# Performance work log

Measured on AMD Instinct MI355X. Metric: run time of the kernel, lower is better.

## Reference

```python
import jax, jax.numpy as jnp
import numpy as np

SLOPE = 5.0                # surrogate gradient slope (SurrogateGradient default)
REFRACTORY_PERIOD = 2.0    # config.refractory_period
ADAPT_DECAY = 0.9          # threshold_adapt EMA decay
ADAPT_INC = 0.1


@jax.custom_vjp
def spike_fn(membrane, threshold):
    # Heaviside spike with surrogate gradient (fast sigmoid), matching SurrogateGradient
    return (membrane >= threshold).astype(membrane.dtype)

def _spike_fwd(membrane, threshold):
    return spike_fn(membrane, threshold), (membrane, threshold)

def _spike_bwd(res, g):
    membrane, threshold = res
    s = jax.nn.sigmoid(SLOPE * (membrane - threshold))
    grad_m = g * SLOPE * s * (1.0 - s)
    # torch returns None (zero) grad for threshold through the spike op itself
    return grad_m, jnp.zeros_like(threshold)

spike_fn.defvjp(_spike_fwd, _spike_bwd)


def setup_inputs() -> dict:
    key = jax.random.key(0)
    kx, = jax.random.split(key, 1)
    B, S, D = 16, 2048, 1024
    x = jax.random.normal(kx, (B, S, D), dtype=jnp.float32)
    beta_mem = jnp.asarray(0.9, dtype=jnp.float32)                      # membrane_decay
    beta_syn = jnp.exp(jnp.asarray(-1.0 / 5.0, dtype=jnp.float32))      # exp(-1/tau_syn)
    threshold_adapt_p = jnp.full((1,), 0.1, dtype=jnp.float32)          # nn.Parameter ones(1)*0.1
    threshold_scale = jnp.ones((D,), dtype=jnp.float32)
    learnable_threshold = jnp.ones((D,), dtype=jnp.float32)             # threshold=1.0
    return {
        "x": x,
        "beta_mem": beta_mem,
        "beta_syn": beta_syn,
        "threshold_adapt_p": threshold_adapt_p,
        "threshold_scale": threshold_scale,
        "learnable_threshold": learnable_threshold,
    }


def _lif(x, beta_mem, beta_syn, threshold_adapt_p, threshold_scale, learnable_threshold):
    B, S, D = x.shape
    z = jnp.zeros((B, D), dtype=x.dtype)
    init = (z, z, z, z)  # membrane, synaptic, threshold_adapt, refractory

    def step(carry, xt):  # xt: (B, D)
        membrane, synaptic, th_adapt, refractory = carry
        synaptic = beta_syn * synaptic + xt
        non_refractory = (refractory <= 0).astype(x.dtype)
        membrane = beta_mem * membrane + synaptic * non_refractory
        cur_th = learnable_threshold + threshold_adapt_p * th_adapt * threshold_scale
        spikes = spike_fn(membrane, cur_th)
        membrane = membrane - spikes * cur_th  # reset_mode='subtract'
        th_adapt = ADAPT_DECAY * th_adapt + ADAPT_INC * spikes
        refractory = jnp.where(
            spikes > 0.5,
            jnp.full_like(spikes, REFRACTORY_PERIOD),
            jnp.clip(refractory - 1.0, 0.0),
        )
        return (membrane, synaptic, th_adapt, refractory), spikes

    carry, spikes = jax.lax.scan(step, init, jnp.swapaxes(x, 0, 1))  # scan over seq
    spike_train = jnp.swapaxes(spikes, 0, 1)  # (B, S, D)
    return spike_train, carry


def reference(x, beta_mem, beta_syn, threshold_adapt_p, threshold_scale, learnable_threshold):
    spike_train, (membrane, synaptic, th_adapt, refractory) = _lif(
        x, beta_mem, beta_syn, threshold_adapt_p, threshold_scale, learnable_threshold
    )
    return spike_train, membrane, synaptic, th_adapt, refractory
```

## Files before the change

### kernel.cpp

```cpp
#include <hip/hip_runtime.h>
#include <stdint.h>


#define SB 16
#define SS 2048
#define SD 1024
#define TILE 64
#define NT (SS / TILE)

typedef const __attribute__((address_space(1))) void* gas_ptr;
typedef __attribute__((address_space(3))) void* las_ptr;

__global__ __launch_bounds__(128, 1) void lif_kernel(
    const float* __restrict__ x,
    const float* __restrict__ beta_mem_p,
    const float* __restrict__ beta_syn_p,
    const float* __restrict__ adapt_p,
    const float* __restrict__ scale_p,
    const float* __restrict__ lth_p,
    float* __restrict__ out)
{
#pragma clang fp contract(off)
    __shared__ __attribute__((aligned(16))) float xbuf[3][TILE][64];
    __shared__ float sbuf[2][64][TILE + 1];

    const int bk = blockIdx.x;
    const int b  = bk >> 4;
    const int d0 = (bk & 15) << 6;

    if (threadIdx.x < 64) {
        const int lane = threadIdx.x;
        const int d    = d0 + lane;

        const float beta_mem = beta_mem_p[0];
        const float beta_syn = beta_syn_p[0];
        const float p        = adapt_p[0];
        const float scale    = scale_p[d];
        const float lth      = lth_p[d];

        float mem = 0.f, syn = 0.f, tha = 0.f;
        bool  nref = true;
        bool  f1 = false, f2 = false;

        __syncthreads();

        int cbuf = 0;
        for (int k = 0; k < NT; ++k) {
            const int sb = k & 1;

            float xa[16], xbv[16], xc[16], xd[16];
            #pragma unroll
            for (int i = 0; i < 16; ++i) xa[i]  = xbuf[cbuf][i][lane];
            #pragma unroll
            for (int i = 0; i < 16; ++i) xbv[i] = xbuf[cbuf][16 + i][lane];
            #pragma unroll
            for (int i = 0; i < 16; ++i) xc[i]  = xbuf[cbuf][32 + i][lane];
            #pragma unroll
            for (int i = 0; i < 16; ++i) xd[i]  = xbuf[cbuf][48 + i][lane];

            auto step = [&](float xt, int ti) {
                syn = __builtin_fmaf(beta_syn, syn, xt);
                const float syn_eff = nref ? syn : 0.f;
                mem = __builtin_fmaf(beta_mem, mem, syn_eff);
                const float q      = p * tha;
                const float cur_th = __builtin_fmaf(q, scale, lth);
                const bool  fired  = (mem >= cur_th);
                const float spike  = fired ? 1.f : 0.f;
                mem = mem - (fired ? cur_th : 0.f);
                tha = __builtin_fmaf(0.9f, tha, fired ? 0.1f : 0.f);
                nref = !(fired || f1);
                f2 = f1; f1 = fired;
                sbuf[sb][lane][ti] = spike;
            };

            #pragma unroll
            for (int i = 0; i < 16; ++i) step(xa[i], i);
            #pragma unroll
            for (int i = 0; i < 16; ++i) step(xbv[i], 16 + i);
            #pragma unroll
            for (int i = 0; i < 16; ++i) step(xc[i], 32 + i);
            #pragma unroll
            for (int i = 0; i < 16; ++i) step(xd[i], 48 + i);

            __syncthreads();
            cbuf = (cbuf == 2) ? 0 : cbuf + 1;
        }

        const float refr = f1 ? 2.0f : (f2 ? 1.0f : 0.0f);
        const size_t base = (size_t)SB * SS * SD;
        const size_t off  = (size_t)b * SD + d;
        out[base + 0 * (size_t)SB * SD + off] = mem;
        out[base + 1 * (size_t)SB * SD + off] = syn;
        out[base + 2 * (size_t)SB * SD + off] = tha;
        out[base + 3 * (size_t)SB * SD + off] = refr;
    } else {
        const int hl = threadIdx.x - 64;

        const float* xb   = x   + ((size_t)b * SS) * SD + d0;
        float*       outb = out + ((size_t)b * SS) * SD + d0;

        const int srow = hl >> 4;
        const int scol = (hl & 15) << 2;
        const float* src_base = xb + (size_t)srow * SD + scol;

        auto issue_tile = [&](int k, int buf) {
            const float* s0 = src_base + (size_t)(k * TILE) * SD;
            float* dst = &xbuf[buf][0][0];
            #pragma unroll
            for (int r = 0; r < 16; ++r) {
                __builtin_amdgcn_global_load_lds(
                    (gas_ptr)(s0 + (size_t)(r * 4) * SD),
                    (las_ptr)(dst + r * 4 * 64),
                    16, 0, 0);
            }
        };

        auto store_tile = [&](int tk) {
            const int sb = tk & 1;
            int idx = tk * TILE * SD + hl;
            #pragma unroll 8
            for (int t = 0; t < TILE; ++t) {
                outb[idx] = sbuf[sb][hl][t];
                idx += SD;
            }
        };

        issue_tile(0, 0);
        issue_tile(1, 1);
        __syncthreads();

        int nbuf = 2;
        for (int k = 0; k < NT; ++k) {
            if (k + 2 < NT) {
                issue_tile(k + 2, nbuf);
                nbuf = (nbuf == 2) ? 0 : nbuf + 1;
            }
            if (k >= 1) store_tile(k - 1);
            __syncthreads();
        }
        store_tile(NT - 1);
    }
}

extern "C" void kernel_launch(void* const* d_in, const int* in_sizes, int n_in,
                              void* d_out, int out_size, void* d_ws, size_t ws_size,
                              hipStream_t stream) {
    const float* x        = (const float*)d_in[0];
    const float* beta_mem = (const float*)d_in[1];
    const float* beta_syn = (const float*)d_in[2];
    const float* adapt_p  = (const float*)d_in[3];
    const float* scale    = (const float*)d_in[4];
    const float* lth      = (const float*)d_in[5];
    float* out = (float*)d_out;

    lif_kernel<<<256, 128, 0, stream>>>(x, beta_mem, beta_syn, adapt_p, scale, lth, out);
}
```

Before: 79.49 us.

## Run two interleaved LIF chains per lane and store spikes directly from compute wave

Each compute lane now advances two independent neuron chains, giving the scan instruction-level parallelism across adjacent D columns. The grid is halved to 128 blocks of 128 columns each. The LDS spike staging buffer and the loader wave's store loop are removed, so the compute wave writes float2 spikes straight to global memory. The loader adds explicit vmcnt waits before barriers. This trades half the blocks (fewer CUs in use on a 256-CU part) for more ILP per serial chain, and it puts global stores on the critical compute wave.

```diff
diff --git a/kernel.cpp b/kernel.cpp
--- a/kernel.cpp
+++ b/kernel.cpp
@@ -11,6 +11,12 @@
 typedef const __attribute__((address_space(1))) void* gas_ptr;
 typedef __attribute__((address_space(3))) void* las_ptr;
 
+struct Chain {
+    float mem, syn, tha;
+    bool  nref, f1, f2;
+    float scale, lth;
+};
+
 __global__ __launch_bounds__(128, 1) void lif_kernel(
     const float* __restrict__ x,
     const float* __restrict__ beta_mem_p,
@@ -21,112 +27,100 @@
     float* __restrict__ out)
 {
 #pragma clang fp contract(off)
-    __shared__ __attribute__((aligned(16))) float xbuf[3][TILE][64];
-    __shared__ float sbuf[2][64][TILE + 1];
+    __shared__ __attribute__((aligned(16))) float xbuf[3][TILE][128];
 
     const int bk = blockIdx.x;
-    const int b  = bk >> 4;
-    const int d0 = (bk & 15) << 6;
+    const int b  = bk >> 3;
+    const int d0 = (bk & 7) << 7;
 
     if (threadIdx.x < 64) {
         const int lane = threadIdx.x;
-        const int d    = d0 + lane;
+        const int dA   = d0 + 2 * lane;
+        const int dB   = dA + 1;
 
         const float beta_mem = beta_mem_p[0];
         const float beta_syn = beta_syn_p[0];
         const float p        = adapt_p[0];
-        const float scale    = scale_p[d];
-        const float lth      = lth_p[d];
 
-        float mem = 0.f, syn = 0.f, tha = 0.f;
-        bool  nref = true;
-        bool  f1 = false, f2 = false;
+        Chain c0{0.f, 0.f, 0.f, true, false, false, scale_p[dA], lth_p[dA]};
+        Chain c1{0.f, 0.f, 0.f, true, false, false, scale_p[dB], lth_p[dB]};
+
+        float2* out2 = (float2*)(out + ((size_t)b * SS) * SD + d0);
+        int sidx = lane;
+
+        auto step = [&](float xt, Chain& c) -> float {
+            c.syn = __builtin_fmaf(beta_syn, c.syn, xt);
+            const float syn_eff = c.nref ? c.syn : 0.f;
+            c.mem = __builtin_fmaf(beta_mem, c.mem, syn_eff);
+            const float q      = p * c.tha;
+            const float cur_th = __builtin_fmaf(q, c.scale, c.lth);
+            const bool  fired  = (c.mem >= cur_th);
+            const float spike  = fired ? 1.f : 0.f;
+            c.mem = c.mem - (fired ? cur_th : 0.f);
+            c.tha = __builtin_fmaf(0.9f, c.tha, fired ? 0.1f : 0.f);
+            c.nref = !(fired || c.f1);
+            c.f2 = c.f1; c.f1 = fired;
+            return spike;
+        };
 
         __syncthreads();
 
         int cbuf = 0;
         for (int k = 0; k < NT; ++k) {
-            const int sb = k & 1;
-
-            float xa[16], xbv[16], xc[16], xd[16];
+            float2 xa[16];
             #pragma unroll
-            for (int i = 0; i < 16; ++i) xa[i]  = xbuf[cbuf][i][lane];
-            #pragma unroll
-            for (int i = 0; i < 16; ++i) xbv[i] = xbuf[cbuf][16 + i][lane];
-            #pragma unroll
-            for (int i = 0; i < 16; ++i) xc[i]  = xbuf[cbuf][32 + i][lane];
-            #pragma unroll
-            for (int i = 0; i < 16; ++i) xd[i]  = xbuf[cbuf][48 + i][lane];
-
-            auto step = [&](float xt, int ti) {
-                syn = __builtin_fmaf(beta_syn, syn, xt);
-                const float syn_eff = nref ? syn : 0.f;
-                mem = __builtin_fmaf(beta_mem, mem, syn_eff);
-                const float q      = p * tha;
-                const float cur_th = __builtin_fmaf(q, scale, lth);
-                const bool  fired  = (mem >= cur_th);
-                const float spike  = fired ? 1.f : 0.f;
-                mem = mem - (fired ? cur_th : 0.f);
-                tha = __builtin_fmaf(0.9f, tha, fired ? 0.1f : 0.f);
-                nref = !(fired || f1);
-                f2 = f1; f1 = fired;
-                sbuf[sb][lane][ti] = spike;
-            };
-
-            #pragma unroll
-            for (int i = 0; i < 16; ++i) step(xa[i], i);
-            #pragma unroll
-            for (int i = 0; i < 16; ++i) step(xbv[i], 16 + i);
-            #pragma unroll
-            for (int i = 0; i < 16; ++i) step(xc[i], 32 + i);
-            #pragma unroll
-            for (int i = 0; i < 16; ++i) step(xd[i], 48 + i);
-
+            for (int g = 0; g < 4; ++g) {
+                #pragma unroll
+                for (int i = 0; i < 16; ++i)
+                    xa[i] = *(const float2*)&xbuf[cbuf][g * 16 + i][2 * lane];
+                #pragma unroll
+                for (int i = 0; i < 16; ++i) {
+                    float2 sv;
+                    sv.x = step(xa[i].x, c0);
+                    sv.y = step(xa[i].y, c1);
+                    out2[sidx] = sv;
+                    sidx += SD / 2;
+                }
+            }
             __syncthreads();
             cbuf = (cbuf == 2) ? 0 : cbuf + 1;
         }
 
-        const float refr = f1 ? 2.0f : (f2 ? 1.0f : 0.0f);
+        const float r0 = c0.f1 ? 2.0f : (c0.f2 ? 1.0f : 0.0f);
+        const float r1 = c1.f1 ? 2.0f : (c1.f2 ? 1.0f : 0.0f);
         const size_t base = (size_t)SB * SS * SD;
-        const size_t off  = (size_t)b * SD + d;
-        out[base + 0 * (size_t)SB * SD + off] = mem;
-        out[base + 1 * (size_t)SB * SD + off] = syn;
-        out[base + 2 * (size_t)SB * SD + off] = tha;
-        out[base + 3 * (size_t)SB * SD + off] = refr;
+        const size_t row  = (size_t)b * SD + d0;
+        float2* m2 = (float2*)(out + base + 0 * (size_t)SB * SD + row);
+        float2* s2 = (float2*)(out + base + 1 * (size_t)SB * SD + row);
+        float2* t2 = (float2*)(out + base + 2 * (size_t)SB * SD + row);
+        float2* r2 = (float2*)(out + base + 3 * (size_t)SB * SD + row);
+        m2[lane] = make_float2(c0.mem, c1.mem);
+        s2[lane] = make_float2(c0.syn, c1.syn);
+        t2[lane] = make_float2(c0.tha, c1.tha);
+        r2[lane] = make_float2(r0, r1);
     } else {
         const int hl = threadIdx.x - 64;
 
-        const float* xb   = x   + ((size_t)b * SS) * SD + d0;
-        float*       outb = out + ((size_t)b * SS) * SD + d0;
-
-        const int srow = hl >> 4;
-        const int scol = (hl & 15) << 2;
-        const float* src_base = xb + (size_t)srow * SD + scol;
+        const int trow = hl >> 5;
+        const int dcol = (hl & 31) << 2;
+        const float* src_base =
+            x + ((size_t)b * SS) * SD + d0 + (size_t)trow * SD + dcol;
 
         auto issue_tile = [&](int k, int buf) {
             const float* s0 = src_base + (size_t)(k * TILE) * SD;
             float* dst = &xbuf[buf][0][0];
             #pragma unroll
-            for (int r = 0; r < 16; ++r) {
+            for (int r = 0; r < 32; ++r) {
                 __builtin_amdgcn_global_load_lds(
-                    (gas_ptr)(s0 + (size_t)(r * 4) * SD),
-                    (las_ptr)(dst + r * 4 * 64),
+                    (gas_ptr)(s0 + (size_t)(2 * r) * SD),
+                    (las_ptr)(dst + r * 2 * 128),
                     16, 0, 0);
-            }
-        };
-
-        auto store_tile = [&](int tk) {
-            const int sb = tk & 1;
-            int idx = tk * TILE * SD + hl;
-            #pragma unroll 8
-            for (int t = 0; t < TILE; ++t) {
-                outb[idx] = sbuf[sb][hl][t];
-                idx += SD;
             }
         };
 
         issue_tile(0, 0);
         issue_tile(1, 1);
+        asm volatile("s_waitcnt vmcnt(0)" ::: "memory");
         __syncthreads();
 
         int nbuf = 2;
@@ -134,11 +128,10 @@
             if (k + 2 < NT) {
                 issue_tile(k + 2, nbuf);
                 nbuf = (nbuf == 2) ? 0 : nbuf + 1;
+                asm volatile("s_waitcnt vmcnt(0)" ::: "memory");
             }
-            if (k >= 1) store_tile(k - 1);
             __syncthreads();
         }
-        store_tile(NT - 1);
     }
 }
 
@@ -153,5 +146,5 @@
     const float* lth      = (const float*)d_in[5];
     float* out = (float*)d_out;
 
-    lif_kernel<<<256, 128, 0, stream>>>(x, beta_mem, beta_syn, adapt_p, scale, lth, out);
+    lif_kernel<<<128, 128, 0, stream>>>(x, beta_mem, beta_syn, adapt_p, scale, lth, out);
 }
```

Result: slower. 108.9 us (+37.0%).
